# Kernel optimization log

Measured on AMD Instinct MI355X. Metric: run time of the kernel, lower is better.

## Reference

```python
import jax, jax.numpy as jnp
import numpy as np

ALPHA = 0.2            # LeakyReLU negative slope
NEG_BIG = -9e15        # mask fill value from the original code


def setup_inputs() -> dict:
    key = jax.random.key(0)
    k1, k2, k3, k4 = jax.random.split(key, 4)
    N, F_in, F_out = 8192, 512, 256
    x = jax.random.normal(k1, (N, F_in), dtype=jnp.float32)
    support = jax.random.randint(k2, (N, N), 0, 2, dtype=jnp.int32)  # dense 0/1 adjacency
    W = jax.random.normal(k3, (F_in, F_out), dtype=jnp.float32) * (1.0 / np.sqrt(F_in))
    a = jax.random.normal(k4, (2 * F_out, 1), dtype=jnp.float32) * 0.05
    return {"x": x, "support": support, "W": W, "a": a}


def _attention_logits(h, a):
    # Faithful reproduction of the ORIGINAL (buggy) torch layout:
    #   a_input = cat([h.repeat(1,N).view(N*N,-1), h.repeat(N,1)], dim=0).view(N, N, 2F)
    # Working out the flat-index arithmetic (N even):
    #   for i <  N/2: a_input[i,j] = concat(h[q], h[q]),  q = 2*i + (j >= N/2)
    #   for i >= N/2: a_input[i,j] = concat(h[(2j) % N], h[(2j+1) % N])   (independent of i)
    # so e_raw[i,j] = a_input[i,j] @ a decomposes via s = h@a1, t = h@a2.
    N, F = h.shape
    a1 = a[:F, 0]
    a2 = a[F:, 0]
    s = h @ a1                     # (N,)
    t = h @ a2                     # (N,)
    u = s + t
    half = N // 2
    j = jnp.arange(N)
    i_top = jnp.arange(half)
    q = 2 * i_top[:, None] + (j[None, :] >= half).astype(jnp.int32)  # (half, N)
    top = u[q]                                                       # rows i < N/2
    bot = s[(2 * j) % N] + t[(2 * j + 1) % N]                        # (N,) same for all i >= N/2
    e_raw = jnp.concatenate([top, jnp.broadcast_to(bot, (N - half, N))], axis=0)
    return jnp.where(e_raw > 0, e_raw, ALPHA * e_raw)  # LeakyReLU


def reference(x, support, W, a):
    h = x @ W                                  # (N, F_out)
    e = _attention_logits(h, a)                # (N, N)
    scores = jnp.where(support > 0, e, jnp.float32(NEG_BIG))
    attn = jax.nn.softmax(scores, axis=1)      # dropout p=0.0 -> identity
    h_out = attn @ h                           # (N, F_out)
    return jax.nn.elu(h_out)                   # concat=True
```

## Files before the change

kernel.cpp:

```cpp
#include <hip/hip_runtime.h>


typedef short bf16x8 __attribute__((ext_vector_type(8)));
typedef float f32x4 __attribute__((ext_vector_type(4)));

static __device__ __forceinline__ unsigned short f2bf(float f) {
    unsigned int u = __builtin_bit_cast(unsigned int, f);
    unsigned int r = (u + 0x7FFFu + ((u >> 16) & 1u)) >> 16;
    return (unsigned short)r;
}
static __device__ __forceinline__ float bf2f(unsigned short s) {
    unsigned int u = ((unsigned int)s) << 16;
    return __builtin_bit_cast(float, u);
}
static __device__ __forceinline__ void glds16(const unsigned short* g, unsigned short* l) {
    __builtin_amdgcn_global_load_lds(
        (const __attribute__((address_space(1))) unsigned int*)(g),
        (__attribute__((address_space(3))) unsigned int*)(l), 16, 0, 0);
}

__global__ __launch_bounds__(256) void k_cvt_x(const float* __restrict__ x,
                                               unsigned short* __restrict__ xb) {
    int i = (blockIdx.x * 256 + threadIdx.x) * 4;
    float4 v = *(const float4*)(x + i);
    ushort4 o = make_ushort4(f2bf(v.x), f2bf(v.y), f2bf(v.z), f2bf(v.w));
    *(ushort4*)(xb + i) = o;
}

__global__ __launch_bounds__(256) void k_cvt_w(const float* __restrict__ W,
                                               unsigned short* __restrict__ Wbt) {
    int idx = blockIdx.x * 256 + threadIdx.x;
    int n = idx >> 9, k = idx & 511;
    Wbt[idx] = f2bf(W[k * 256 + n]);
}

__global__ __launch_bounds__(256) void k_gemm_h(const unsigned short* __restrict__ xb,
                                                const unsigned short* __restrict__ Wbt,
                                                unsigned short* __restrict__ h,
                                                unsigned short* __restrict__ B1t) {
    __shared__ unsigned short Asm[128][72];
    __shared__ unsigned short Bsm[64][72];
    int tid = threadIdx.x;
    int wv = tid >> 6, ln = tid & 63;
    int m0 = blockIdx.x * 128, n0 = blockIdx.y * 64;

    f32x4 acc[2][4];
#pragma unroll
    for (int i = 0; i < 2; i++)
#pragma unroll
        for (int j = 0; j < 4; j++) acc[i][j] = (f32x4)0.0f;

    for (int k0 = 0; k0 < 512; k0 += 64) {
        {
            int r = tid >> 1, c = (tid & 1) * 32;
            const unsigned short* src = xb + (m0 + r) * 512 + k0 + c;
            *(bf16x8*)&Asm[r][c]      = *(const bf16x8*)(src);
            *(bf16x8*)&Asm[r][c + 8]  = *(const bf16x8*)(src + 8);
            *(bf16x8*)&Asm[r][c + 16] = *(const bf16x8*)(src + 16);
            *(bf16x8*)&Asm[r][c + 24] = *(const bf16x8*)(src + 24);
        }
        {
            int r = tid >> 2, c = (tid & 3) * 16;
            const unsigned short* src = Wbt + (n0 + r) * 512 + k0 + c;
            *(bf16x8*)&Bsm[r][c]     = *(const bf16x8*)(src);
            *(bf16x8*)&Bsm[r][c + 8] = *(const bf16x8*)(src + 8);
        }
        __syncthreads();
        int lr = ln & 15, lk = (ln >> 4) * 8;
#pragma unroll
        for (int ks = 0; ks < 2; ks++) {
            int kk = ks * 32 + lk;
            bf16x8 a0 = *(const bf16x8*)&Asm[wv * 32 + lr][kk];
            bf16x8 a1 = *(const bf16x8*)&Asm[wv * 32 + 16 + lr][kk];
#pragma unroll
            for (int nt = 0; nt < 4; nt++) {
                bf16x8 b = *(const bf16x8*)&Bsm[nt * 16 + lr][kk];
                acc[0][nt] = __builtin_amdgcn_mfma_f32_16x16x32_bf16(a0, b, acc[0][nt], 0, 0, 0);
                acc[1][nt] = __builtin_amdgcn_mfma_f32_16x16x32_bf16(a1, b, acc[1][nt], 0, 0, 0);
            }
        }
        __syncthreads();
    }
    int lr = ln & 15, lrow = (ln >> 4) * 4;
#pragma unroll
    for (int mt = 0; mt < 2; mt++) {
#pragma unroll
        for (int nt = 0; nt < 4; nt++) {
            int mg = m0 + wv * 32 + mt * 16 + lrow;
            int ng = n0 + nt * 16 + lr;
            ushort4 tb = make_ushort4(f2bf(acc[mt][nt][0]), f2bf(acc[mt][nt][1]),
                                      f2bf(acc[mt][nt][2]), f2bf(acc[mt][nt][3]));
            h[(mg + 0) * 256 + ng] = tb.x;
            h[(mg + 1) * 256 + ng] = tb.y;
            h[(mg + 2) * 256 + ng] = tb.z;
            h[(mg + 3) * 256 + ng] = tb.w;
            *(ushort4*)&B1t[ng * 8192 + mg] = tb;
        }
    }
}

__global__ __launch_bounds__(256) void k_st(const unsigned short* __restrict__ h,
                                            const float* __restrict__ a,
                                            float* __restrict__ s, float* __restrict__ t) {
    int wv = threadIdx.x >> 6, ln = threadIdx.x & 63;
    int j = blockIdx.x * 4 + wv;
    ushort4 hv = *(const ushort4*)(h + j * 256 + ln * 4);
    float4 a1 = *(const float4*)(a + ln * 4);
    float4 a2 = *(const float4*)(a + 256 + ln * 4);
    float s_ = bf2f(hv.x) * a1.x + bf2f(hv.y) * a1.y + bf2f(hv.z) * a1.z + bf2f(hv.w) * a1.w;
    float t_ = bf2f(hv.x) * a2.x + bf2f(hv.y) * a2.y + bf2f(hv.z) * a2.z + bf2f(hv.w) * a2.w;
#pragma unroll
    for (int off = 32; off; off >>= 1) {
        s_ += __shfl_down(s_, off);
        t_ += __shfl_down(t_, off);
    }
    if (ln == 0) { s[j] = s_; t[j] = t_; }
}

__global__ __launch_bounds__(256) void k_weights(const float* __restrict__ s,
                                                 const float* __restrict__ t,
                                                 float* __restrict__ wb,
                                                 float* __restrict__ eL,
                                                 float* __restrict__ eR,
                                                 unsigned short* __restrict__ B1t) {
    int j = blockIdx.x * 256 + threadIdx.x;
    float eb = s[(2 * j) & 8191] + t[(2 * j + 1) & 8191];
    eb = eb > 0.0f ? eb : 0.2f * eb;
    wb[j] = expf(eb);
    if (j < 4096) {
        float cL = s[2 * j] + t[2 * j];
        cL = cL > 0.0f ? cL : 0.2f * cL;
        float cR = s[2 * j + 1] + t[2 * j + 1];
        cR = cR > 0.0f ? cR : 0.2f * cR;
        eL[j] = expf(cL);
        eR[j] = expf(cR);
    }
    B1t[256 * 8192 + j] = 0x3F80;
#pragma unroll
    for (int f = 257; f < 272; f++) B1t[f * 8192 + j] = 0;
}

__global__ __launch_bounds__(256) void k_b2(const unsigned short* __restrict__ B1t,
                                            const float* __restrict__ wb,
                                            unsigned short* __restrict__ B2t) {
    int j = blockIdx.x * 256 + threadIdx.x;
    int f = blockIdx.y;
    B2t[f * 8192 + j] = f2bf(wb[j] * bf2f(B1t[f * 8192 + j]));
}

static __device__ __forceinline__ bf16x8 cvt01(int4 a, int4 b) {
    bf16x8 r;
    r[0] = a.x ? (short)0x3F80 : (short)0; r[1] = a.y ? (short)0x3F80 : (short)0;
    r[2] = a.z ? (short)0x3F80 : (short)0; r[3] = a.w ? (short)0x3F80 : (short)0;
    r[4] = b.x ? (short)0x3F80 : (short)0; r[5] = b.y ? (short)0x3F80 : (short)0;
    r[6] = b.z ? (short)0x3F80 : (short)0; r[7] = b.w ? (short)0x3F80 : (short)0;
    return r;
}

__global__ __launch_bounds__(256, 4) void k_mgemm(const int* __restrict__ sup,
                                                  const unsigned short* __restrict__ B1t,
                                                  const unsigned short* __restrict__ B2t,
                                                  float* __restrict__ P) {
    __shared__ unsigned short Bsm[2 * 8704];
    int tid = threadIdx.x, wv = tid >> 6, ln = tid & 63;
    int bid = blockIdx.x;
    int q = bid & 7;
    int strip = bid >> 3;
    long K0 = (long)q * 1024;
    long m0 = (long)strip * 64;
    const unsigned short* Bt = (strip < 64) ? B1t : B2t;

    const unsigned short* sp0; const unsigned short* sp1;
    const unsigned short* sp2; const unsigned short* sp3;
    const unsigned short* sp4;
    int cb0, cb1, cb2, cb3, cb4;
    {
        int ch;
#define SETUP_SP(I, SP, CB) \
        ch = (I)*256 + wv*64 + ln; \
        { int row = ch >> 2, c = ch & 3; \
          CB = ((I)*256 + wv*64) * 8; \
          SP = Bt + (long)row * 8192 + K0 + ((c ^ (row & 3)) << 3); }
        SETUP_SP(0, sp0, cb0)
        SETUP_SP(1, sp1, cb1)
        SETUP_SP(2, sp2, cb2)
        SETUP_SP(3, sp3, cb3)
        ch = 1024 + ln;
        { int row = ch >> 2, c = ch & 3;
          cb4 = 1024 * 8;
          sp4 = Bt + (long)row * 8192 + K0 + ((c ^ (row & 3)) << 3); }
#undef SETUP_SP
    }

    const int* ap = sup + (m0 + wv * 16 + (ln & 15)) * 8192 + K0 + (ln >> 4) * 8;

    f32x4 acc[17];
#pragma unroll
    for (int i = 0; i < 17; i++) acc[i] = (f32x4)0.0f;

    {
        unsigned short* dst = Bsm;
        glds16(sp0, dst + cb0);
        glds16(sp1, dst + cb1);
        glds16(sp2, dst + cb2);
        glds16(sp3, dst + cb3);
        if (wv == 0) glds16(sp4, dst + cb4);
    }
    int4 c0 = *(const int4*)(ap);
    int4 c1 = *(const int4*)(ap + 4);
    int4 n0 = *(const int4*)(ap + 32);
    int4 n1 = *(const int4*)(ap + 36);
    int4 f0 = c0, f1 = c1;
    asm volatile("s_waitcnt vmcnt(4)" ::: "memory");
    __builtin_amdgcn_s_barrier();

    int lr = ln & 15;
    int swz16 = 16 * ((ln >> 4) ^ (ln & 3));

#pragma unroll 1
    for (int it = 0; it < 32; ++it) {
        int buf = it & 1;
        if (it < 31) {
            unsigned short* dst = Bsm + (buf ^ 1) * 8704;
            glds16(sp0 + (it + 1) * 32, dst + cb0);
            glds16(sp1 + (it + 1) * 32, dst + cb1);
            glds16(sp2 + (it + 1) * 32, dst + cb2);
            glds16(sp3 + (it + 1) * 32, dst + cb3);
            if (wv == 0) glds16(sp4 + (it + 1) * 32, dst + cb4);
        }
        if (it < 30) {
            f0 = *(const int4*)(ap + (it + 2) * 32);
            f1 = *(const int4*)(ap + (it + 2) * 32 + 4);
        }
        bf16x8 av = cvt01(c0, c1);
        const char* base = (const char*)Bsm + buf * 17408 + 64 * lr + swz16;
#pragma unroll
        for (int f = 0; f < 17; f++) {
            bf16x8 bv = *(const bf16x8*)(base + f * 1024);
            acc[f] = __builtin_amdgcn_mfma_f32_16x16x32_bf16(av, bv, acc[f], 0, 0, 0);
        }
        c0 = n0; c1 = n1; n0 = f0; n1 = f1;
        if (it < 31) {
            if (it < 30) asm volatile("s_waitcnt vmcnt(2)" ::: "memory");
            else         asm volatile("s_waitcnt vmcnt(0)" ::: "memory");
            __builtin_amdgcn_s_barrier();
        }
    }

    long grow = m0 + wv * 16 + (ln >> 4) * 4;
    float* op = P + ((long)q * 8192 + grow) * 272 + lr;
#pragma unroll
    for (int f = 0; f < 17; f++)
#pragma unroll
        for (int r = 0; r < 4; r++)
            op[(long)r * 272 + f * 16] = acc[f][r];
}

__global__ __launch_bounds__(256) void k_out(const float* __restrict__ P,
                                             const float* __restrict__ eL,
                                             const float* __restrict__ eR,
                                             float* __restrict__ outp) {
    int i = blockIdx.x, f = threadIdx.x;
    const float* p = P + (long)i * 272;
    const long QS = 8192l * 272;
    float num, den;
    if (i < 4096) {
        float tln = 0, trn = 0, tld = 0, trd = 0;
#pragma unroll
        for (int q = 0; q < 4; q++) { tln += p[q * QS + f]; tld += p[q * QS + 256]; }
#pragma unroll
        for (int q = 4; q < 8; q++) { trn += p[q * QS + f]; trd += p[q * QS + 256]; }
        float el = eL[i], er = eR[i];
        num = el * tln + er * trn;
        den = el * tld + er * trd;
    } else {
        num = 0; den = 0;
#pragma unroll
        for (int q = 0; q < 8; q++) { num += p[q * QS + f]; den += p[q * QS + 256]; }
    }
    float r = num / den;
    outp[(long)i * 256 + f] = r > 0.0f ? r : expm1f(r);
}

extern "C" void kernel_launch(void* const* d_in, const int* in_sizes, int n_in,
                              void* d_out, int out_size, void* d_ws, size_t ws_size,
                              hipStream_t stream) {
    (void)in_sizes; (void)n_in; (void)out_size; (void)ws_size;
    const float* x = (const float*)d_in[0];
    const int* sup = (const int*)d_in[1];
    const float* W = (const float*)d_in[2];
    const float* a = (const float*)d_in[3];
    float* outp = (float*)d_out;

    char* ws = (char*)d_ws;
    size_t off = 0;
    auto alloc = [&](size_t bytes) -> void* {
        void* p = ws + off;
        off += (bytes + 255) & ~(size_t)255;
        return p;
    };
    unsigned short* xb  = (unsigned short*)alloc(8192 * 512 * 2);
    unsigned short* Wbt = (unsigned short*)alloc(256 * 512 * 2);
    unsigned short* h   = (unsigned short*)alloc(8192 * 256 * 2);
    unsigned short* B1t = (unsigned short*)alloc(272 * 8192 * 2);
    unsigned short* B2t = (unsigned short*)alloc(272 * 8192 * 2);
    float* s   = (float*)alloc(8192 * 4);
    float* t   = (float*)alloc(8192 * 4);
    float* wb  = (float*)alloc(8192 * 4);
    float* eL  = (float*)alloc(4096 * 4);
    float* eR  = (float*)alloc(4096 * 4);
    float* P   = (float*)alloc((size_t)8 * 8192 * 272 * 4);

    k_cvt_x<<<4096, 256, 0, stream>>>(x, xb);
    k_cvt_w<<<512, 256, 0, stream>>>(W, Wbt);
    k_gemm_h<<<dim3(64, 4), 256, 0, stream>>>(xb, Wbt, h, B1t);
    k_st<<<2048, 256, 0, stream>>>(h, a, s, t);
    k_weights<<<32, 256, 0, stream>>>(s, t, wb, eL, eR, B1t);
    k_b2<<<dim3(32, 272), 256, 0, stream>>>(B1t, wb, B2t);
    k_mgemm<<<1024, 256, 0, stream>>>(sup, B1t, B2t, P);
    k_out<<<8192, 256, 0, stream>>>(P, eL, eR, outp);
}
```

Baseline: 186.5 us.

## Double M-tile per wave in masked GEMM and deepen B staging to four buffers

Each block now covers 128 rows instead of 64, with every wave computing two 16-row MFMA tiles that share each B fragment read from LDS. This halves LDS B traffic and global B loads per output row. B staging goes from double-buffered to a 4-deep ring with prefetch three iterations ahead, so waitcnt and barrier placement change. The cost is double the accumulator registers and LDS, which drops occupancy (launch bounds 4 to 2) and halves the grid to 512 blocks.

```diff
diff --git a/kernel.cpp b/kernel.cpp
--- a/kernel.cpp
+++ b/kernel.cpp
@@ -157,61 +157,66 @@
     return r;
 }
 
-__global__ __launch_bounds__(256, 4) void k_mgemm(const int* __restrict__ sup,
+__global__ __launch_bounds__(256, 2) void k_mgemm(const int* __restrict__ sup,
                                                   const unsigned short* __restrict__ B1t,
                                                   const unsigned short* __restrict__ B2t,
                                                   float* __restrict__ P) {
-    __shared__ unsigned short Bsm[2 * 8704];
+    __shared__ unsigned short Bsm[4 * 8704];
     int tid = threadIdx.x, wv = tid >> 6, ln = tid & 63;
     int bid = blockIdx.x;
     int q = bid & 7;
     int strip = bid >> 3;
     long K0 = (long)q * 1024;
-    long m0 = (long)strip * 64;
-    const unsigned short* Bt = (strip < 64) ? B1t : B2t;
-
-    const unsigned short* sp0; const unsigned short* sp1;
-    const unsigned short* sp2; const unsigned short* sp3;
-    const unsigned short* sp4;
-    int cb0, cb1, cb2, cb3, cb4;
+    long m0 = (long)strip * 128;
+    const unsigned short* Bt = (strip < 32) ? B1t : B2t;
+
+    const unsigned short* sp[5];
+    int cb[5];
+#pragma unroll
+    for (int i = 0; i < 4; i++) {
+        int ch = i * 256 + wv * 64 + ln;
+        int row = ch >> 2, c = ch & 3;
+        cb[i] = (i * 256 + wv * 64) * 8;
+        sp[i] = Bt + (long)row * 8192 + K0 + ((c ^ (row & 3)) << 3);
+    }
     {
-        int ch;
-#define SETUP_SP(I, SP, CB) \
-        ch = (I)*256 + wv*64 + ln; \
-        { int row = ch >> 2, c = ch & 3; \
-          CB = ((I)*256 + wv*64) * 8; \
-          SP = Bt + (long)row * 8192 + K0 + ((c ^ (row & 3)) << 3); }
-        SETUP_SP(0, sp0, cb0)
-        SETUP_SP(1, sp1, cb1)
-        SETUP_SP(2, sp2, cb2)
-        SETUP_SP(3, sp3, cb3)
-        ch = 1024 + ln;
-        { int row = ch >> 2, c = ch & 3;
-          cb4 = 1024 * 8;
-          sp4 = Bt + (long)row * 8192 + K0 + ((c ^ (row & 3)) << 3); }
-#undef SETUP_SP
-    }
-
-    const int* ap = sup + (m0 + wv * 16 + (ln & 15)) * 8192 + K0 + (ln >> 4) * 8;
-
-    f32x4 acc[17];
-#pragma unroll
-    for (int i = 0; i < 17; i++) acc[i] = (f32x4)0.0f;
-
-    {
-        unsigned short* dst = Bsm;
-        glds16(sp0, dst + cb0);
-        glds16(sp1, dst + cb1);
-        glds16(sp2, dst + cb2);
-        glds16(sp3, dst + cb3);
-        if (wv == 0) glds16(sp4, dst + cb4);
-    }
-    int4 c0 = *(const int4*)(ap);
-    int4 c1 = *(const int4*)(ap + 4);
-    int4 n0 = *(const int4*)(ap + 32);
-    int4 n1 = *(const int4*)(ap + 36);
-    int4 f0 = c0, f1 = c1;
-    asm volatile("s_waitcnt vmcnt(4)" ::: "memory");
+        int ch = 1024 + wv * 16 + (ln & 15);
+        int row = ch >> 2, c = ch & 3;
+        cb[4] = (1024 + wv * 16) * 8;
+        sp[4] = Bt + (long)row * 8192 + K0 + ((c ^ (row & 3)) << 3);
+    }
+
+    const int* ap0 = sup + (m0 + wv * 32 + (ln & 15)) * 8192 + K0 + (ln >> 4) * 8;
+    const int* ap1 = ap0 + 16 * 8192;
+
+    f32x4 acc[2][17];
+#pragma unroll
+    for (int i = 0; i < 2; i++)
+#pragma unroll
+        for (int j = 0; j < 17; j++) acc[i][j] = (f32x4)0.0f;
+
+#define STAGE_B(T) do {                                              \
+        unsigned short* dst_ = Bsm + ((T) & 3) * 8704;               \
+        long ko_ = (long)(T) * 32;                                   \
+        glds16(sp[0] + ko_, dst_ + cb[0]);                           \
+        glds16(sp[1] + ko_, dst_ + cb[1]);                           \
+        glds16(sp[2] + ko_, dst_ + cb[2]);                           \
+        glds16(sp[3] + ko_, dst_ + cb[3]);                           \
+        if (ln < 16) glds16(sp[4] + ko_, dst_ + cb[4]);              \
+    } while (0)
+
+    int4 c0, c1, c2, c3;
+    int4 n0, n1, n2, n3;
+    int4 g0, g1, g2, g3;
+
+    STAGE_B(0);
+    c0 = *(const int4*)(ap0); c1 = *(const int4*)(ap0 + 4);
+    c2 = *(const int4*)(ap1); c3 = *(const int4*)(ap1 + 4);
+    STAGE_B(1);
+    n0 = *(const int4*)(ap0 + 32); n1 = *(const int4*)(ap0 + 36);
+    n2 = *(const int4*)(ap1 + 32); n3 = *(const int4*)(ap1 + 36);
+    STAGE_B(2);
+    asm volatile("s_waitcnt vmcnt(14)" ::: "memory");
     __builtin_amdgcn_s_barrier();
 
     int lr = ln & 15;
@@ -219,41 +224,48 @@
 
 #pragma unroll 1
     for (int it = 0; it < 32; ++it) {
-        int buf = it & 1;
-        if (it < 31) {
-            unsigned short* dst = Bsm + (buf ^ 1) * 8704;
-            glds16(sp0 + (it + 1) * 32, dst + cb0);
-            glds16(sp1 + (it + 1) * 32, dst + cb1);
-            glds16(sp2 + (it + 1) * 32, dst + cb2);
-            glds16(sp3 + (it + 1) * 32, dst + cb3);
-            if (wv == 0) glds16(sp4 + (it + 1) * 32, dst + cb4);
-        }
         if (it < 30) {
-            f0 = *(const int4*)(ap + (it + 2) * 32);
-            f1 = *(const int4*)(ap + (it + 2) * 32 + 4);
-        }
-        bf16x8 av = cvt01(c0, c1);
-        const char* base = (const char*)Bsm + buf * 17408 + 64 * lr + swz16;
+            const int* a0 = ap0 + (it + 2) * 32;
+            const int* a1 = ap1 + (it + 2) * 32;
+            g0 = *(const int4*)(a0); g1 = *(const int4*)(a0 + 4);
+            g2 = *(const int4*)(a1); g3 = *(const int4*)(a1 + 4);
+        }
+        if (it < 29) STAGE_B(it + 3);
+
+        bf16x8 av0 = cvt01(c0, c1);
+        bf16x8 av1 = cvt01(c2, c3);
+        const char* base = (const char*)Bsm + (it & 3) * 17408 + 64 * lr + swz16;
 #pragma unroll
         for (int f = 0; f < 17; f++) {
             bf16x8 bv = *(const bf16x8*)(base + f * 1024);
-            acc[f] = __builtin_amdgcn_mfma_f32_16x16x32_bf16(av, bv, acc[f], 0, 0, 0);
-        }
-        c0 = n0; c1 = n1; n0 = f0; n1 = f1;
-        if (it < 31) {
-            if (it < 30) asm volatile("s_waitcnt vmcnt(2)" ::: "memory");
-            else         asm volatile("s_waitcnt vmcnt(0)" ::: "memory");
+            acc[0][f] = __builtin_amdgcn_mfma_f32_16x16x32_bf16(av0, bv, acc[0][f], 0, 0, 0);
+            acc[1][f] = __builtin_amdgcn_mfma_f32_16x16x32_bf16(av1, bv, acc[1][f], 0, 0, 0);
+        }
+        c0 = n0; c1 = n1; c2 = n2; c3 = n3;
+        n0 = g0; n1 = g1; n2 = g2; n3 = g3;
+
+        if (it < 29) {
+            asm volatile("s_waitcnt vmcnt(14)" ::: "memory");
             __builtin_amdgcn_s_barrier();
-        }
-    }
-
-    long grow = m0 + wv * 16 + (ln >> 4) * 4;
+        } else if (it == 29) {
+            asm volatile("s_waitcnt vmcnt(9)" ::: "memory");
+            __builtin_amdgcn_s_barrier();
+        } else if (it == 30) {
+            asm volatile("s_waitcnt vmcnt(0)" ::: "memory");
+            __builtin_amdgcn_s_barrier();
+        }
+    }
+#undef STAGE_B
+
+    long grow = m0 + wv * 32 + (ln >> 4) * 4;
     float* op = P + ((long)q * 8192 + grow) * 272 + lr;
 #pragma unroll
-    for (int f = 0; f < 17; f++)
-#pragma unroll
-        for (int r = 0; r < 4; r++)
-            op[(long)r * 272 + f * 16] = acc[f][r];
+    for (int mf = 0; mf < 2; mf++)
+#pragma unroll
+        for (int f = 0; f < 17; f++)
+#pragma unroll
+            for (int r = 0; r < 4; r++)
+                op[(long)(mf * 16 + r) * 272 + f * 16] = acc[mf][f][r];
 }
 
 __global__ __launch_bounds__(256) void k_out(const float* __restrict__ P,
@@ -317,6 +329,6 @@
     k_st<<<2048, 256, 0, stream>>>(h, a, s, t);
     k_weights<<<32, 256, 0, stream>>>(s, t, wb, eL, eR, B1t);
     k_b2<<<dim3(32, 272), 256, 0, stream>>>(B1t, wb, B2t);
-    k_mgemm<<<1024, 256, 0, stream>>>(sup, B1t, B2t, P);
+    k_mgemm<<<512, 256, 0, stream>>>(sup, B1t, B2t, P);
     k_out<<<8192, 256, 0, stream>>>(P, eL, eR, outp);
 }
```

Result: faster. 171.1 us (-8.2%).
